# Performance work log

Hardware: AMD Instinct MI355X
Metric: run time of the kernel (lower is better)

The kernel has to match this reference:

```python
import jax, jax.numpy as jnp
import numpy as np

BS, N, D_IN, HID, D_OUT = 16, 256, 128, 128, 128


def setup_inputs() -> dict:
    key = jax.random.key(0)
    ks = jax.random.split(key, 10)
    s = 0.02
    return {
        "x": jax.random.normal(ks[0], (BS, N, D_IN), dtype=jnp.float32),
        "adj": jax.random.randint(ks[1], (BS, N, N), 0, 2, dtype=jnp.int32),
        "W_fc": jax.random.normal(ks[2], (D_IN, HID), dtype=jnp.float32) * s,
        "b_fc": jnp.zeros((HID,), dtype=jnp.float32),
        "W_a1": jax.random.normal(ks[3], (2 * HID, HID), dtype=jnp.float32) * s,
        "b_a1": jnp.zeros((HID,), dtype=jnp.float32),
        "w_a2": jax.random.normal(ks[4], (HID,), dtype=jnp.float32) * s,
        "b_a2": jnp.zeros((), dtype=jnp.float32),
        "W_out": jax.random.normal(ks[5], (HID, D_OUT), dtype=jnp.float32) * s,
        "b_out": jnp.zeros((D_OUT,), dtype=jnp.float32),
    }


def reference(x, adj, W_fc, b_fc, W_a1, b_a1, w_a2, b_a2, W_out, b_out):
    # h = fc(x): (bs, n, hid)
    h = jnp.einsum("bnd,dh->bnh", x, W_fc) + b_fc
    # attn first layer on concat([h_i, h_j]) decomposes into two half-projections
    # (same math as Linear(2*hid, hid) on the concatenated pair features).
    a_i = jnp.einsum("bnh,hk->bnk", h, W_a1[:HID])  # contribution of h_i
    a_j = jnp.einsum("bnh,hk->bnk", h, W_a1[HID:])  # contribution of h_j
    pre = a_i[:, :, None, :] + a_j[:, None, :, :] + b_a1  # (bs, n, n, hid)
    e = jnp.einsum("bijk,k->bij", jax.nn.relu(pre), w_a2) + b_a2  # (bs, n, n)
    e = jnp.where(adj == 0, jnp.float32(-1e9), e)
    attn = jax.nn.softmax(e, axis=-1)
    h_prime = jnp.einsum("bij,bjh->bih", attn, h)
    out = jnp.einsum("bih,ho->bio", h_prime, W_out) + b_out
    return out
```

## Files before the change

### kernel.cpp

```cpp
#include <hip/hip_runtime.h>

#define BS  16
#define NN  256
#define HID 128

__device__ __forceinline__ int xcd_swz(int bid) {
    return (bid & 7) * 64 + (bid >> 3);
}

__global__ __launch_bounds__(512, 4) void gat_k1(
    const float* __restrict__ x, const float* __restrict__ W_fc,
    const float* __restrict__ b_fc, const float* __restrict__ W_a1,
    const float* __restrict__ b_a1, const float* __restrict__ W_out,
    float* __restrict__ aiT, float* __restrict__ ajT, float* __restrict__ g)
{
    __shared__ __align__(16) float xs[8][HID];
    __shared__ __align__(16) float hs[8][HID];
    __shared__ __align__(16) float red[4][8][HID];

    const int tid = threadIdx.x;
    const int k   = tid & 127;
    const int q   = tid >> 7;
    const int swz = xcd_swz(blockIdx.x);
    const int r0  = swz * 8;
    const int b   = r0 >> 8;
    const int n0  = r0 & 255;

    for (int t = tid; t < 8 * HID; t += 512)
        xs[t >> 7][t & 127] = x[r0 * HID + t];
    __syncthreads();

    {
        float acc[8] = {0,0,0,0,0,0,0,0};
        const int dq = 32 * q;
        #pragma unroll 2
        for (int d = 0; d < 32; d += 4) {
            float w[4];
            #pragma unroll
            for (int t = 0; t < 4; ++t) w[t] = W_fc[(dq + d + t) * HID + k];
            #pragma unroll
            for (int r = 0; r < 8; ++r) {
                const float4 xv = *(const float4*)&xs[r][dq + d];
                acc[r] += xv.x * w[0] + xv.y * w[1] + xv.z * w[2] + xv.w * w[3];
            }
        }
        #pragma unroll
        for (int r = 0; r < 8; ++r) red[q][r][k] = acc[r];
    }
    __syncthreads();

    {
        const float bf = b_fc[k];
        #pragma unroll
        for (int r2 = 0; r2 < 2; ++r2) {
            const int r = 2 * q + r2;
            hs[r][k] = (red[0][r][k] + red[1][r][k])
                     + (red[2][r][k] + red[3][r][k]) + bf;
        }
    }
    __syncthreads();

    {
        const int is_aj = q >> 1;
        const int half  = q & 1;
        const float* Wp = W_a1 + (is_aj * HID + half * 64) * HID;
        float acc[8] = {0,0,0,0,0,0,0,0};
        const int hb = half * 64;
        #pragma unroll 2
        for (int d = 0; d < 64; d += 4) {
            float w[4];
            #pragma unroll
            for (int t = 0; t < 4; ++t) w[t] = Wp[(d + t) * HID + k];
            #pragma unroll
            for (int r = 0; r < 8; ++r) {
                const float4 hv = *(const float4*)&hs[r][hb + d];
                acc[r] += hv.x * w[0] + hv.y * w[1] + hv.z * w[2] + hv.w * w[3];
            }
        }
        #pragma unroll
        for (int r = 0; r < 8; ++r) red[q][r][k] = acc[r];
    }
    __syncthreads();

    {
        const int is_aj = q >> 1;
        const int rb4   = (q & 1) * 4;
        const float bias = is_aj ? 0.f : b_a1[k];
        const int p0 = 2 * is_aj, p1 = 2 * is_aj + 1;
        float4 v;
        v.x = red[p0][rb4 + 0][k] + red[p1][rb4 + 0][k] + bias;
        v.y = red[p0][rb4 + 1][k] + red[p1][rb4 + 1][k] + bias;
        v.z = red[p0][rb4 + 2][k] + red[p1][rb4 + 2][k] + bias;
        v.w = red[p0][rb4 + 3][k] + red[p1][rb4 + 3][k] + bias;
        float* dst = (is_aj ? ajT : aiT) + (b * HID + k) * NN + n0 + rb4;
        *(float4*)dst = v;
    }
    __syncthreads();

    {
        float acc[8] = {0,0,0,0,0,0,0,0};
        const int dq = 32 * q;
        #pragma unroll 2
        for (int d = 0; d < 32; d += 4) {
            float w[4];
            #pragma unroll
            for (int t = 0; t < 4; ++t) w[t] = W_out[(dq + d + t) * HID + k];
            #pragma unroll
            for (int r = 0; r < 8; ++r) {
                const float4 hv = *(const float4*)&hs[r][dq + d];
                acc[r] += hv.x * w[0] + hv.y * w[1] + hv.z * w[2] + hv.w * w[3];
            }
        }
        #pragma unroll
        for (int r = 0; r < 8; ++r) red[q][r][k] = acc[r];
    }
    __syncthreads();

    {
        #pragma unroll
        for (int r2 = 0; r2 < 2; ++r2) {
            const int r = 2 * q + r2;
            g[(r0 + r) * HID + k] = (red[0][r][k] + red[1][r][k])
                                  + (red[2][r][k] + red[3][r][k]);
        }
    }
}

__global__ __launch_bounds__(512, 4) void gat_k2(
    const float* __restrict__ aiT, const float* __restrict__ ajT,
    const float* __restrict__ g,  const int* __restrict__ adj,
    const float* __restrict__ w_a2, const float* __restrict__ b_a2,
    const float* __restrict__ b_out, float* __restrict__ out)
{
    __shared__ __align__(16) float aiw[HID][8];
    __shared__ __align__(16) float w2s[HID];
    __shared__ __align__(16) float ep[8][NN];
    __shared__ __align__(16) float red[4][8][HID];

    const int tid = threadIdx.x;
    const int swz = xcd_swz(blockIdx.x);
    const int b   = swz >> 5;
    const int i0  = (swz & 31) * 8;
    const int wv  = tid >> 6, lane = tid & 63;

    for (int t = tid; t < HID * 8; t += 512) {
        const int kk = t >> 3, r = t & 7;
        aiw[kk][r] = aiT[(b * HID + kk) * NN + i0 + r];
    }
    if (tid < HID) w2s[tid] = w_a2[tid];
    __syncthreads();

    const int jj = 32 * wv + (lane & 31);
    const int rg = lane >> 5;
    {
        int am[4];
        #pragma unroll
        for (int r = 0; r < 4; ++r)
            am[r] = adj[(b * NN + i0 + 4 * rg + r) * NN + jj];

        const float* ajp = ajT + b * HID * NN + jj;
        float acc[4] = {0.f, 0.f, 0.f, 0.f};
        float saw = 0.f;
        #pragma unroll 8
        for (int kk = 0; kk < HID; ++kk) {
            const float a   = ajp[kk * NN];
            const float4 f4 = *(const float4*)&aiw[kk][4 * rg];
            const float wk  = w2s[kk];
            saw = __builtin_fmaf(a, wk, saw);
            acc[0] = __builtin_fmaf(fmaxf(f4.x, -a), wk, acc[0]);
            acc[1] = __builtin_fmaf(fmaxf(f4.y, -a), wk, acc[1]);
            acc[2] = __builtin_fmaf(fmaxf(f4.z, -a), wk, acc[2]);
            acc[3] = __builtin_fmaf(fmaxf(f4.w, -a), wk, acc[3]);
        }
        const float base = saw + b_a2[0];
        #pragma unroll
        for (int r = 0; r < 4; ++r)
            ep[4 * rg + r][jj] = am[r] ? acc[r] + base : -1e9f;
    }
    __syncthreads();

    {
        float4 e4 = *(const float4*)&ep[wv][4 * lane];
        float m = fmaxf(fmaxf(e4.x, e4.y), fmaxf(e4.z, e4.w));
        #pragma unroll
        for (int off = 32; off; off >>= 1) m = fmaxf(m, __shfl_xor(m, off));
        const float p0 = __expf(e4.x - m), p1 = __expf(e4.y - m);
        const float p2 = __expf(e4.z - m), p3 = __expf(e4.w - m);
        float s = (p0 + p1) + (p2 + p3);
        #pragma unroll
        for (int off = 32; off; off >>= 1) s += __shfl_xor(s, off);
        const float inv = 1.f / s;
        const float4 pv = {p0 * inv, p1 * inv, p2 * inv, p3 * inv};
        *(float4*)&ep[wv][4 * lane] = pv;
    }
    __syncthreads();

    const int k = tid & 127, qh = tid >> 7;
    {
        float o[8] = {0,0,0,0,0,0,0,0};
        const float* gb = g + (b * NN + qh * 64) * HID + k;
        const int jb = qh * 64;
        #pragma unroll 2
        for (int jq = 0; jq < 64; jq += 4) {
            const float g0 = gb[(jq + 0) * HID];
            const float g1 = gb[(jq + 1) * HID];
            const float g2 = gb[(jq + 2) * HID];
            const float g3 = gb[(jq + 3) * HID];
            #pragma unroll
            for (int r = 0; r < 8; ++r) {
                const float4 pv = *(const float4*)&ep[r][jb + jq];
                o[r] += pv.x * g0 + pv.y * g1 + pv.z * g2 + pv.w * g3;
            }
        }
        #pragma unroll
        for (int r = 0; r < 8; ++r) red[qh][r][k] = o[r];
    }
    __syncthreads();

    {
        const float bo = b_out[k];
        #pragma unroll
        for (int r2 = 0; r2 < 2; ++r2) {
            const int r = 2 * qh + r2;
            out[(b * NN + i0 + r) * HID + k] =
                (red[0][r][k] + red[1][r][k]) +
                (red[2][r][k] + red[3][r][k]) + bo;
        }
    }
}

extern "C" void kernel_launch(void* const* d_in, const int* in_sizes, int n_in,
                              void* d_out, int out_size, void* d_ws, size_t ws_size,
                              hipStream_t stream) {
    const float* x     = (const float*)d_in[0];
    const int*   adj   = (const int*)  d_in[1];
    const float* W_fc  = (const float*)d_in[2];
    const float* b_fc  = (const float*)d_in[3];
    const float* W_a1  = (const float*)d_in[4];
    const float* b_a1  = (const float*)d_in[5];
    const float* w_a2  = (const float*)d_in[6];
    const float* b_a2  = (const float*)d_in[7];
    const float* W_out = (const float*)d_in[8];
    const float* b_out = (const float*)d_in[9];
    float* out = (float*)d_out;

    float* ws  = (float*)d_ws;
    float* aiT = ws;
    float* ajT = ws + BS * NN * HID;
    float* g   = ws + 2 * BS * NN * HID;

    gat_k1<<<BS * NN / 8, 512, 0, stream>>>(x, W_fc, b_fc, W_a1, b_a1, W_out,
                                            aiT, ajT, g);
    gat_k2<<<BS * (NN / 8), 512, 0, stream>>>(aiT, ajT, g, adj, w_a2, b_a2,
                                              b_out, out);
}
```

Before: 42.41 us.

## Split feature projection into separate kernel and drop LDS split-K reductions

The first kernel is split in two. One kernel computes h = x·W_fc and writes it to a new workspace buffer. A second kernel reads h back and computes the attention half-projections and the W_out projection. Each thread now computes full dot products over all 128 inputs for a few rows, reading rows straight from global memory. This removes the shared-memory staging, the split-K partial sums and the block barriers, at the cost of an extra kernel launch, a round trip of h through global memory, and more redundant row and weight loads per thread.

```diff
diff --git a/kernel.cpp b/kernel.cpp
--- a/kernel.cpp
+++ b/kernel.cpp
@@ -8,16 +8,44 @@
     return (bid & 7) * 64 + (bid >> 3);
 }
 
-__global__ __launch_bounds__(512, 4) void gat_k1(
+__global__ __launch_bounds__(512, 4) void gat_k1a(
     const float* __restrict__ x, const float* __restrict__ W_fc,
-    const float* __restrict__ b_fc, const float* __restrict__ W_a1,
+    const float* __restrict__ b_fc, float* __restrict__ h)
+{
+    const int tid = threadIdx.x;
+    const int k   = tid & 127;
+    const int q   = tid >> 7;
+    const int swz = xcd_swz(blockIdx.x);
+    const int r0  = swz * 8;
+
+    const float* xr0 = x + (r0 + 2 * q) * HID;
+    const float* xr1 = xr0 + HID;
+
+    const float bf = b_fc[k];
+    float a0a = bf, a0b = 0.f, a1a = 0.f, a1b = 0.f;
+    #pragma unroll 4
+    for (int d0 = 0; d0 < HID; d0 += 8) {
+        float w[8];
+        #pragma unroll
+        for (int t = 0; t < 8; ++t) w[t] = W_fc[(d0 + t) * HID + k];
+        const float4 x00 = *(const float4*)(xr0 + d0);
+        const float4 x01 = *(const float4*)(xr0 + d0 + 4);
+        const float4 x10 = *(const float4*)(xr1 + d0);
+        const float4 x11 = *(const float4*)(xr1 + d0 + 4);
+        a0a += x00.x * w[0] + x00.y * w[1] + x00.z * w[2] + x00.w * w[3];
+        a0b += x01.x * w[4] + x01.y * w[5] + x01.z * w[6] + x01.w * w[7];
+        a1a += x10.x * w[0] + x10.y * w[1] + x10.z * w[2] + x10.w * w[3];
+        a1b += x11.x * w[4] + x11.y * w[5] + x11.z * w[6] + x11.w * w[7];
+    }
+    h[(r0 + 2 * q + 0) * HID + k] = a0a + a0b;
+    h[(r0 + 2 * q + 1) * HID + k] = a1a + a1b;
+}
+
+__global__ __launch_bounds__(512, 4) void gat_k1b(
+    const float* __restrict__ h, const float* __restrict__ W_a1,
     const float* __restrict__ b_a1, const float* __restrict__ W_out,
     float* __restrict__ aiT, float* __restrict__ ajT, float* __restrict__ g)
 {
-    __shared__ __align__(16) float xs[8][HID];
-    __shared__ __align__(16) float hs[8][HID];
-    __shared__ __align__(16) float red[4][8][HID];
-
     const int tid = threadIdx.x;
     const int k   = tid & 127;
     const int q   = tid >> 7;
@@ -26,103 +54,56 @@
     const int b   = r0 >> 8;
     const int n0  = r0 & 255;
 
-    for (int t = tid; t < 8 * HID; t += 512)
-        xs[t >> 7][t & 127] = x[r0 * HID + t];
-    __syncthreads();
-
-    {
-        float acc[8] = {0,0,0,0,0,0,0,0};
-        const int dq = 32 * q;
-        #pragma unroll 2
-        for (int d = 0; d < 32; d += 4) {
+    {
+        const int is_aj = q >> 1;
+        const int rb    = (q & 1) * 4;
+        const float* Wp = W_a1 + is_aj * HID * HID;
+        const float bias = is_aj ? 0.f : b_a1[k];
+        const float* hr0 = h + (r0 + rb + 0) * HID;
+        const float* hr1 = h + (r0 + rb + 1) * HID;
+        const float* hr2 = h + (r0 + rb + 2) * HID;
+        const float* hr3 = h + (r0 + rb + 3) * HID;
+
+        float acc[4] = {bias, bias, bias, bias};
+        #pragma unroll 4
+        for (int d0 = 0; d0 < HID; d0 += 4) {
             float w[4];
             #pragma unroll
-            for (int t = 0; t < 4; ++t) w[t] = W_fc[(dq + d + t) * HID + k];
+            for (int t = 0; t < 4; ++t) w[t] = Wp[(d0 + t) * HID + k];
+            const float4 h0 = *(const float4*)(hr0 + d0);
+            const float4 h1 = *(const float4*)(hr1 + d0);
+            const float4 h2 = *(const float4*)(hr2 + d0);
+            const float4 h3 = *(const float4*)(hr3 + d0);
+            acc[0] += h0.x * w[0] + h0.y * w[1] + h0.z * w[2] + h0.w * w[3];
+            acc[1] += h1.x * w[0] + h1.y * w[1] + h1.z * w[2] + h1.w * w[3];
+            acc[2] += h2.x * w[0] + h2.y * w[1] + h2.z * w[2] + h2.w * w[3];
+            acc[3] += h3.x * w[0] + h3.y * w[1] + h3.z * w[2] + h3.w * w[3];
+        }
+        const float4 v = {acc[0], acc[1], acc[2], acc[3]};
+        float* dst = (is_aj ? ajT : aiT) + (b * HID + k) * NN + n0 + rb;
+        *(float4*)dst = v;
+    }
+
+    {
+        const float* gr0 = h + (r0 + 2 * q) * HID;
+        const float* gr1 = gr0 + HID;
+        float o0a = 0.f, o0b = 0.f, o1a = 0.f, o1b = 0.f;
+        #pragma unroll 4
+        for (int d0 = 0; d0 < HID; d0 += 8) {
+            float w[8];
             #pragma unroll
-            for (int r = 0; r < 8; ++r) {
-                const float4 xv = *(const float4*)&xs[r][dq + d];
-                acc[r] += xv.x * w[0] + xv.y * w[1] + xv.z * w[2] + xv.w * w[3];
-            }
-        }
-        #pragma unroll
-        for (int r = 0; r < 8; ++r) red[q][r][k] = acc[r];
-    }
-    __syncthreads();
-
-    {
-        const float bf = b_fc[k];
-        #pragma unroll
-        for (int r2 = 0; r2 < 2; ++r2) {
-            const int r = 2 * q + r2;
-            hs[r][k] = (red[0][r][k] + red[1][r][k])
-                     + (red[2][r][k] + red[3][r][k]) + bf;
-        }
-    }
-    __syncthreads();
-
-    {
-        const int is_aj = q >> 1;
-        const int half  = q & 1;
-        const float* Wp = W_a1 + (is_aj * HID + half * 64) * HID;
-        float acc[8] = {0,0,0,0,0,0,0,0};
-        const int hb = half * 64;
-        #pragma unroll 2
-        for (int d = 0; d < 64; d += 4) {
-            float w[4];
-            #pragma unroll
-            for (int t = 0; t < 4; ++t) w[t] = Wp[(d + t) * HID + k];
-            #pragma unroll
-            for (int r = 0; r < 8; ++r) {
-                const float4 hv = *(const float4*)&hs[r][hb + d];
-                acc[r] += hv.x * w[0] + hv.y * w[1] + hv.z * w[2] + hv.w * w[3];
-            }
-        }
-        #pragma unroll
-        for (int r = 0; r < 8; ++r) red[q][r][k] = acc[r];
-    }
-    __syncthreads();
-
-    {
-        const int is_aj = q >> 1;
-        const int rb4   = (q & 1) * 4;
-        const float bias = is_aj ? 0.f : b_a1[k];
-        const int p0 = 2 * is_aj, p1 = 2 * is_aj + 1;
-        float4 v;
-        v.x = red[p0][rb4 + 0][k] + red[p1][rb4 + 0][k] + bias;
-        v.y = red[p0][rb4 + 1][k] + red[p1][rb4 + 1][k] + bias;
-        v.z = red[p0][rb4 + 2][k] + red[p1][rb4 + 2][k] + bias;
-        v.w = red[p0][rb4 + 3][k] + red[p1][rb4 + 3][k] + bias;
-        float* dst = (is_aj ? ajT : aiT) + (b * HID + k) * NN + n0 + rb4;
-        *(float4*)dst = v;
-    }
-    __syncthreads();
-
-    {
-        float acc[8] = {0,0,0,0,0,0,0,0};
-        const int dq = 32 * q;
-        #pragma unroll 2
-        for (int d = 0; d < 32; d += 4) {
-            float w[4];
-            #pragma unroll
-            for (int t = 0; t < 4; ++t) w[t] = W_out[(dq + d + t) * HID + k];
-            #pragma unroll
-            for (int r = 0; r < 8; ++r) {
-                const float4 hv = *(const float4*)&hs[r][dq + d];
-                acc[r] += hv.x * w[0] + hv.y * w[1] + hv.z * w[2] + hv.w * w[3];
-            }
-        }
-        #pragma unroll
-        for (int r = 0; r < 8; ++r) red[q][r][k] = acc[r];
-    }
-    __syncthreads();
-
-    {
-        #pragma unroll
-        for (int r2 = 0; r2 < 2; ++r2) {
-            const int r = 2 * q + r2;
-            g[(r0 + r) * HID + k] = (red[0][r][k] + red[1][r][k])
-                                  + (red[2][r][k] + red[3][r][k]);
-        }
+            for (int t = 0; t < 8; ++t) w[t] = W_out[(d0 + t) * HID + k];
+            const float4 h00 = *(const float4*)(gr0 + d0);
+            const float4 h01 = *(const float4*)(gr0 + d0 + 4);
+            const float4 h10 = *(const float4*)(gr1 + d0);
+            const float4 h11 = *(const float4*)(gr1 + d0 + 4);
+            o0a += h00.x * w[0] + h00.y * w[1] + h00.z * w[2] + h00.w * w[3];
+            o0b += h01.x * w[4] + h01.y * w[5] + h01.z * w[6] + h01.w * w[7];
+            o1a += h10.x * w[0] + h10.y * w[1] + h10.z * w[2] + h10.w * w[3];
+            o1b += h11.x * w[4] + h11.y * w[5] + h11.z * w[6] + h11.w * w[7];
+        }
+        g[(r0 + 2 * q + 0) * HID + k] = o0a + o0b;
+        g[(r0 + 2 * q + 1) * HID + k] = o1a + o1b;
     }
 }
 
@@ -248,9 +229,11 @@
     float* aiT = ws;
     float* ajT = ws + BS * NN * HID;
     float* g   = ws + 2 * BS * NN * HID;
-
-    gat_k1<<<BS * NN / 8, 512, 0, stream>>>(x, W_fc, b_fc, W_a1, b_a1, W_out,
-                                            aiT, ajT, g);
+    float* hbuf= ws + 3 * BS * NN * HID;
+
+    gat_k1a<<<BS * NN / 8, 512, 0, stream>>>(x, W_fc, b_fc, hbuf);
+    gat_k1b<<<BS * NN / 8, 512, 0, stream>>>(hbuf, W_a1, b_a1, W_out,
+                                             aiT, ajT, g);
     gat_k2<<<BS * (NN / 8), 512, 0, stream>>>(aiT, ajT, g, adj, w_a2, b_a2,
                                               b_out, out);
 }
```

New measurement: 72.51 us. 1.71x slower.
